# Kernel tuning notes

Hardware: AMD Instinct MI355X
Metric: run time of the kernel (lower is better)

Reference implementation:

```python
import jax, jax.numpy as jnp
import numpy as np

B, L, D, H, FF = 2, 2048, 2048, 16, 8192
DH = D // H
NEG = -1e9


def setup_inputs() -> dict:
    key = jax.random.key(0)
    ks = jax.random.split(key, 9)
    x = jax.random.normal(ks[0], (B, L, D), dtype=jnp.float32)
    # additive causal mask, broadcastable to [B, H, L, L]
    causal = jnp.triu(jnp.full((L, L), NEG, dtype=jnp.float32), k=1)
    mask = causal[None, None, :, :]
    s = 1.0 / np.sqrt(D)
    Wq = jax.random.normal(ks[1], (D, D), dtype=jnp.float32) * s
    Wk = jax.random.normal(ks[2], (D, D), dtype=jnp.float32) * s
    Wv = jax.random.normal(ks[3], (D, D), dtype=jnp.float32) * s
    Wo = jax.random.normal(ks[4], (D, D), dtype=jnp.float32) * s
    W_up = jax.random.normal(ks[5], (FF, D), dtype=jnp.float32) * s
    b_up = jnp.zeros((FF,), dtype=jnp.float32)
    W_down = jax.random.normal(ks[6], (D, FF), dtype=jnp.float32) * (1.0 / np.sqrt(FF))
    return {"x": x, "mask": mask, "Wq": Wq, "Wk": Wk, "Wv": Wv, "Wo": Wo,
            "W_up": W_up, "b_up": b_up, "W_down": W_down}


def reference(x, mask, Wq, Wk, Wv, Wo, W_up, b_up, W_down):
    b, l, d = x.shape
    # projections (torch Linear: y = x @ W.T); reshape to [B, H, L, DH]
    q = (x @ Wq.T).reshape(b, l, H, DH).transpose(0, 2, 1, 3)
    k = (x @ Wk.T).reshape(b, l, H, DH).transpose(0, 2, 1, 3)
    v = (x @ Wv.T).reshape(b, l, H, DH).transpose(0, 2, 1, 3)
    # NOTE: original module applies NO 1/sqrt(d_head) scaling
    scores = jnp.einsum('bhqd,bhkd->bhqk', q, k) + mask
    attn = jax.nn.softmax(scores, axis=-1)
    out = jnp.einsum('bhqk,bhkd->bhqd', attn, v)
    out = out.transpose(0, 2, 1, 3).reshape(b, l, d)
    x = x + out @ Wo.T
    h = jax.nn.relu(x @ W_up.T + b_up)
    return x + h @ W_down.T
```

## Files before the change

kernel.cpp:

```cpp
#include <hip/hip_runtime.h>
#include <stdint.h>

typedef _Float16 f16;
typedef __attribute__((ext_vector_type(8))) _Float16 f16x8;
typedef __attribute__((ext_vector_type(4))) _Float16 f16x4;
typedef __attribute__((ext_vector_type(4))) float f32x4;

__device__ __forceinline__ void gload16(void* lds, const void* gc) {
  void* g = const_cast<void*>(gc);
  __builtin_amdgcn_global_load_lds((__attribute__((address_space(1))) void*)g,
                                   (__attribute__((address_space(3))) void*)lds,
                                   16, 0, 0);
}

__global__ __launch_bounds__(256) void k_cast(const float* __restrict__ in,
                                              f16* __restrict__ out, int n4) {
  int stride = gridDim.x * blockDim.x;
  for (int i = blockIdx.x * blockDim.x + threadIdx.x; i < n4; i += stride) {
    float4 v = ((const float4*)in)[i];
    f16x4 o;
    o[0] = (f16)v.x; o[1] = (f16)v.y; o[2] = (f16)v.z; o[3] = (f16)v.w;
    ((f16x4*)out)[i] = o;
  }
}

__global__ __launch_bounds__(256) void k_transpose_v(const f16* __restrict__ vp,
                                                     f16* __restrict__ vt) {
  __shared__ __attribute__((aligned(16))) f16 tile[64][66];
  const int lt = blockIdx.x, dt = blockIdx.y, bh = blockIdx.z;
  const int t = threadIdx.x;
  const int r = t >> 3, c = 8 * (t & 7);
  const f16* src = vp + ((size_t)bh * 2048 + lt * 64) * 128 + dt * 64;
#pragma unroll
  for (int i = 0; i < 2; ++i) {
    union { f16x8 v; unsigned u[4]; } uu;
    uu.v = *(const f16x8*)&src[(size_t)(i * 32 + r) * 128 + c];
#pragma unroll
    for (int j = 0; j < 4; ++j)
      *(unsigned*)&tile[i * 32 + r][c + 2 * j] = uu.u[j];
  }
  __syncthreads();
  f16* dst = vt + ((size_t)bh * 128 + dt * 64) * 2048 + lt * 64;
#pragma unroll
  for (int i = 0; i < 2; ++i) {
    const int dr = i * 32 + r;
    f16x8 o;
#pragma unroll
    for (int e = 0; e < 8; ++e) o[e] = tile[c + e][dr];
    *(f16x8*)&dst[(size_t)dr * 2048 + c] = o;
  }
}

__global__ __launch_bounds__(256) void k_fuseout(const f16* __restrict__ x1b,
                                                 const float* __restrict__ p0,
                                                 const float* __restrict__ p1,
                                                 float* __restrict__ out, int n4) {
  int stride = gridDim.x * blockDim.x;
  for (int i = blockIdx.x * blockDim.x + threadIdx.x; i < n4; i += stride) {
    float4 a = ((const float4*)p0)[i];
    float4 b = ((const float4*)p1)[i];
    f16x4 xb = ((const f16x4*)x1b)[i];
    float4 o;
    o.x = (float)xb[0] + a.x + b.x;
    o.y = (float)xb[1] + a.y + b.y;
    o.z = (float)xb[2] + a.z + b.z;
    o.w = (float)xb[3] + a.w + b.w;
    ((float4*)out)[i] = o;
  }
}

template <int EPI, int SPLITOUT, int BK>
__global__ __launch_bounds__(256, 4) void gemm_nt(const f16* __restrict__ A,
                                                  const f16* __restrict__ B,
                                                  int Kit, int ld, int N,
                                                  const float* __restrict__ res,
                                                  const float* __restrict__ bias,
                                                  float* __restrict__ outf,
                                                  float* __restrict__ outf2,
                                                  f16* __restrict__ outb,
                                                  f16* __restrict__ outb_lo,
                                                  f16* __restrict__ outv) {
  constexpr int TSZ = 128 * BK;
  constexpr int CH  = 2048;
  constexpr int RPC = CH / BK;
  constexpr int NCH = 128 / RPC;
  constexpr int CW  = BK / 8;
  __shared__ __attribute__((aligned(16))) f16 As[TSZ];
  __shared__ __attribute__((aligned(16))) f16 Bs[TSZ];
  const int t = threadIdx.x;
  const int l = t & 63;
  const int w = t >> 6;
  const int wr = w >> 1, wc = w & 1;

  const int nwg = gridDim.x * gridDim.y;
  const int id = blockIdx.y * gridDim.x + blockIdx.x;
  const int sw = (id & 7) * (nwg >> 3) + (id >> 3);
  const int bn = sw % gridDim.x;
  const int bm = sw / gridDim.x;
  const int k0 = blockIdx.z * Kit;

  f32x4 acc[4][4] = {};

  const size_t aoff = (size_t)bm * 128 * ld + k0;
  const size_t boff = (size_t)bn * 128 * ld + k0;

  const int sr = t / CW;
  const int sc = 8 * (t % CW);
  const int lbase = w * 512;

  const int lr = l & 15, lq = l >> 4;
  const int nk = Kit / BK;
  for (int kt = 0; kt < nk; ++kt) {
    const size_t gbase = (size_t)kt * BK + (size_t)sr * ld + sc;
#pragma unroll
    for (int j = 0; j < NCH; ++j) {
      gload16(As + j * CH + lbase, A + aoff + (size_t)j * RPC * ld + gbase);
      gload16(Bs + j * CH + lbase, B + boff + (size_t)j * RPC * ld + gbase);
    }
    __syncthreads();
#pragma unroll
    for (int kk = 0; kk < BK / 32; ++kk) {
      f16x8 af[4], bfr[4];
#pragma unroll
      for (int m = 0; m < 4; ++m)
        af[m] = *(const f16x8*)&As[(wr * 64 + m * 16 + lr) * BK + kk * 32 + 8 * lq];
#pragma unroll
      for (int n = 0; n < 4; ++n)
        bfr[n] = *(const f16x8*)&Bs[(wc * 64 + n * 16 + lr) * BK + kk * 32 + 8 * lq];
#pragma unroll
      for (int m = 0; m < 4; ++m)
#pragma unroll
        for (int n = 0; n < 4; ++n)
          acc[m][n] = __builtin_amdgcn_mfma_f32_16x16x32_f16(af[m], bfr[n], acc[m][n], 0, 0, 0);
    }
    __syncthreads();
  }

  const size_t QKS = (size_t)8 << 20;
#pragma unroll
  for (int m = 0; m < 4; ++m) {
#pragma unroll
    for (int r = 0; r < 4; ++r) {
      const int grow = bm * 128 + wr * 64 + m * 16 + lq * 4 + r;
#pragma unroll
      for (int n = 0; n < 4; ++n) {
        const int gcol = bn * 128 + wc * 64 + n * 16 + lr;
        const float v = acc[m][n][r];
        if constexpr (EPI == 0) {
          const int which = gcol >> 11;
          const int hcol = gcol & 2047;
          const int bb = grow >> 11, ll = grow & 2047;
          const int hh = hcol >> 7, dh = hcol & 127;
          const size_t idx = ((size_t)((bb * 16 + hh) * 2048 + ll) << 7) + dh;
          const f16 hv = (f16)v;
          if (which == 2) {
            outv[idx] = hv;
          } else {
            outb[which * QKS + idx] = hv;
            if constexpr (SPLITOUT) outb_lo[which * QKS + idx] = (f16)(v - (float)hv);
          }
        } else if constexpr (EPI == 1) {
          const size_t idx = (size_t)grow * N + gcol;
          outb[idx] = (f16)(res[idx] + v);
        } else if constexpr (EPI == 2) {
          const size_t idx = (size_t)grow * N + gcol;
          outb[idx] = (f16)fmaxf(v + bias[gcol], 0.f);
        } else {
          const size_t idx = (size_t)grow * N + gcol;
          (blockIdx.z ? outf2 : outf)[idx] = v;
        }
      }
    }
  }
}

__global__ __launch_bounds__(256) void k_attn(const f16* __restrict__ q_hi,
                                              const f16* __restrict__ q_lo,
                                              const f16* __restrict__ k_hi,
                                              const f16* __restrict__ k_lo,
                                              const f16* __restrict__ vtp,
                                              f16* __restrict__ op) {
  __shared__ __attribute__((aligned(16))) f16 Ks_hi[64 * 136];
  __shared__ __attribute__((aligned(16))) f16 Ks_lo[64 * 136];
  __shared__ __attribute__((aligned(16))) f16 Vs[128 * 72];
  __shared__ __attribute__((aligned(16))) f16 Ps[4][16 * 72];
  const int t = threadIdx.x, l = t & 63, w = t >> 6;
  const int qtA = 31 - (int)blockIdx.x;
  const int qtB = (int)blockIdx.x;
  const int bh = blockIdx.y;
  const int qA0 = qtA * 64, qB0 = qtB * 64;
  const int lr = l & 15, lq = l >> 4;

  const f16* qhp = q_hi + (size_t)bh * 2048 * 128;
  const f16* qlp = q_lo + (size_t)bh * 2048 * 128;
  const f16* khp = k_hi + (size_t)bh * 2048 * 128;
  const f16* klp = k_lo + (size_t)bh * 2048 * 128;
  const f16* vhp = vtp + (size_t)bh * 128 * 2048;

  const int krow = t >> 4, kcol8 = 8 * (t & 15);
  const int vrow = t >> 3, vcol8 = 8 * (t & 7);

  f16x8 aqhA[4], aqlA[4], aqhB[4], aqlB[4];
#pragma unroll
  for (int c = 0; c < 4; ++c) {
    const size_t qiA = (size_t)(qA0 + w * 16 + lr) * 128 + c * 32 + 8 * lq;
    const size_t qiB = (size_t)(qB0 + w * 16 + lr) * 128 + c * 32 + 8 * lq;
    aqhA[c] = *(const f16x8*)&qhp[qiA];
    aqlA[c] = *(const f16x8*)&qlp[qiA];
    aqhB[c] = *(const f16x8*)&qhp[qiB];
    aqlB[c] = *(const f16x8*)&qlp[qiB];
  }

  f32x4 accA[8] = {}, accB[8] = {};
  float mrA[4], srA[4], mrB[4], srB[4];
#pragma unroll
  for (int r = 0; r < 4; ++r) {
    mrA[r] = -1e30f; srA[r] = 0.f;
    mrB[r] = -1e30f; srB[r] = 0.f;
  }

  f16x8 kregh[4], kregl[4], vreg[4];
  auto load_tile = [&](int kt) {
#pragma unroll
    for (int i = 0; i < 4; ++i) {
      const size_t ki = (size_t)(kt * 64 + i * 16 + krow) * 128 + kcol8;
      kregh[i] = *(const f16x8*)&khp[ki];
      kregl[i] = *(const f16x8*)&klp[ki];
      vreg[i] = *(const f16x8*)&vhp[(size_t)(i * 32 + vrow) * 2048 + kt * 64 + vcol8];
    }
  };
  load_tile(0);

  auto process = [&](const f16x8 (&aqh)[4], const f16x8 (&aql)[4],
                     f32x4 (&acc)[8], float (&mr)[4], float (&sr)[4],
                     int kt, int qt, int q0) {
    f32x4 s[4];
    __builtin_amdgcn_s_setprio(1);
#pragma unroll
    for (int nt = 0; nt < 4; ++nt) {
      f32x4 zh = {}, zl = {};
#pragma unroll
      for (int kc = 0; kc < 4; ++kc) {
        const int li = (nt * 16 + lr) * 136 + kc * 32 + 8 * lq;
        f16x8 bh_ = *(const f16x8*)&Ks_hi[li];
        f16x8 bl_ = *(const f16x8*)&Ks_lo[li];
        zh = __builtin_amdgcn_mfma_f32_16x16x32_f16(aqh[kc], bh_, zh, 0, 0, 0);
        zl = __builtin_amdgcn_mfma_f32_16x16x32_f16(aql[kc], bh_, zl, 0, 0, 0);
        zl = __builtin_amdgcn_mfma_f32_16x16x32_f16(aqh[kc], bl_, zl, 0, 0, 0);
      }
#pragma unroll
      for (int r = 0; r < 4; ++r) s[nt][r] = zh[r] + zl[r];
    }
    __builtin_amdgcn_s_setprio(0);
    if (kt == qt) {
#pragma unroll
      for (int nt = 0; nt < 4; ++nt)
#pragma unroll
        for (int r = 0; r < 4; ++r) {
          const int key = kt * 64 + nt * 16 + lr;
          const int qr = q0 + w * 16 + lq * 4 + r;
          if (key > qr) s[nt][r] = -1e30f;
        }
    }
    float mnew[4], scale[4], tsum[4];
#pragma unroll
    for (int r = 0; r < 4; ++r) {
      float mx = fmaxf(fmaxf(s[0][r], s[1][r]), fmaxf(s[2][r], s[3][r]));
#pragma unroll
      for (int off = 1; off < 16; off <<= 1)
        mx = fmaxf(mx, __shfl_xor(mx, off));
      mnew[r] = fmaxf(mr[r], mx);
      scale[r] = __expf(mr[r] - mnew[r]);
      mr[r] = mnew[r];
      tsum[r] = 0.f;
    }
#pragma unroll
    for (int nt = 0; nt < 4; ++nt)
#pragma unroll
      for (int r = 0; r < 4; ++r) {
        const float p = __expf(s[nt][r] - mnew[r]);
        tsum[r] += p;
        Ps[w][(lq * 4 + r) * 72 + nt * 16 + lr] = (f16)p;
      }
#pragma unroll
    for (int r = 0; r < 4; ++r) {
      float ts = tsum[r];
#pragma unroll
      for (int off = 1; off < 16; off <<= 1)
        ts += __shfl_xor(ts, off);
      sr[r] = sr[r] * scale[r] + ts;
    }
#pragma unroll
    for (int nt = 0; nt < 8; ++nt)
#pragma unroll
      for (int r = 0; r < 4; ++r)
        acc[nt][r] *= scale[r];
    __builtin_amdgcn_s_setprio(1);
#pragma unroll
    for (int kc = 0; kc < 2; ++kc) {
      f16x8 ap = *(const f16x8*)&Ps[w][lr * 72 + kc * 32 + 8 * lq];
#pragma unroll
      for (int nt = 0; nt < 8; ++nt) {
        f16x8 bv = *(const f16x8*)&Vs[(nt * 16 + lr) * 72 + kc * 32 + 8 * lq];
        acc[nt] = __builtin_amdgcn_mfma_f32_16x16x32_f16(ap, bv, acc[nt], 0, 0, 0);
      }
    }
    __builtin_amdgcn_s_setprio(0);
  };

  for (int kt = 0; kt <= qtA; ++kt) {
    __syncthreads();
#pragma unroll
    for (int i = 0; i < 4; ++i) {
      const int li = (i * 16 + krow) * 136 + kcol8;
      *(f16x8*)&Ks_hi[li] = kregh[i];
      *(f16x8*)&Ks_lo[li] = kregl[i];
      *(f16x8*)&Vs[(i * 32 + vrow) * 72 + vcol8] = vreg[i];
    }
    __syncthreads();
    if (kt < qtA) load_tile(kt + 1);
    process(aqhA, aqlA, accA, mrA, srA, kt, qtA, qA0);
    if (kt <= qtB) process(aqhB, aqlB, accB, mrB, srB, kt, qtB, qB0);
  }

  const int bb = bh >> 4, hh = bh & 15;
  auto wout = [&](f32x4 (&acc)[8], float (&sr)[4], int q0) {
#pragma unroll
    for (int r = 0; r < 4; ++r) {
      const float inv = 1.f / sr[r];
      const size_t row = (size_t)(bb * 2048 + q0 + w * 16 + lq * 4 + r);
#pragma unroll
      for (int nt = 0; nt < 8; ++nt)
        op[row * 2048 + hh * 128 + nt * 16 + lr] = (f16)(acc[nt][r] * inv);
    }
  };
  wout(accA, srA, qA0);
  wout(accB, srB, qB0);
}

extern "C" void kernel_launch(void* const* d_in, const int* in_sizes, int n_in,
                              void* d_out, int out_size, void* d_ws, size_t ws_size,
                              hipStream_t stream) {
  const float* x   = (const float*)d_in[0];
  const float* Wq  = (const float*)d_in[2];
  const float* Wk  = (const float*)d_in[3];
  const float* Wv  = (const float*)d_in[4];
  const float* Wo  = (const float*)d_in[5];
  const float* Wup = (const float*)d_in[6];
  const float* bup = (const float*)d_in[7];
  const float* Wdn = (const float*)d_in[8];
  float* out = (float*)d_out;

  const size_t M1 = 1u << 20;
  f16* W = (f16*)d_ws;
  f16* x_hi    = W + 0 * M1;
  f16* wqkv_hi = W + 8 * M1;
  f16* wo_hi   = W + 20 * M1;
  f16* wup_hi  = W + 24 * M1;
  f16* wdn_hi  = W + 40 * M1;
  f16* q_hi    = W + 56 * M1;
  f16* q_lo    = W + 72 * M1;
  f16* vp      = W + 88 * M1;
  f16* vtb     = W + 96 * M1;
  f16* x1b   = x_hi;
  float* p0  = (float*)(W + 24 * M1);
  f16* hb    = W + 56 * M1;
  float* p1  = (float*)(W + 88 * M1);
  f16* attno = vp;
  if (ws_size < (size_t)104 * M1 * sizeof(f16)) return;

  auto cg = [](size_t n4) { size_t g = (n4 + 255) / 256; return (unsigned)(g > 2048 ? 2048 : g); };
  dim3 b256(256);
  k_cast<<<cg(2 * M1), b256, 0, stream>>>(x, x_hi, (int)(2 * M1));
  k_cast<<<cg(1 * M1), b256, 0, stream>>>(Wq, wqkv_hi, (int)(1 * M1));
  k_cast<<<cg(1 * M1), b256, 0, stream>>>(Wk, wqkv_hi + 4 * M1, (int)(1 * M1));
  k_cast<<<cg(1 * M1), b256, 0, stream>>>(Wv, wqkv_hi + 8 * M1, (int)(1 * M1));
  k_cast<<<cg(1 * M1), b256, 0, stream>>>(Wo, wo_hi, (int)(1 * M1));
  k_cast<<<cg(4 * M1), b256, 0, stream>>>(Wup, wup_hi, (int)(4 * M1));
  k_cast<<<cg(4 * M1), b256, 0, stream>>>(Wdn, wdn_hi, (int)(4 * M1));

  gemm_nt<0, 1, 64><<<dim3(48, 32), b256, 0, stream>>>(
      x_hi, wqkv_hi, 2048, 2048, 6144,
      nullptr, nullptr, nullptr, nullptr, q_hi, q_lo, vp);
  k_transpose_v<<<dim3(32, 2, 32), b256, 0, stream>>>(vp, vtb);
  k_attn<<<dim3(16, 32), b256, 0, stream>>>(
      q_hi, q_lo, q_hi + 8 * M1, q_lo + 8 * M1, vtb, attno);
  gemm_nt<1, 0, 64><<<dim3(16, 32), b256, 0, stream>>>(
      attno, wo_hi, 2048, 2048, 2048,
      x, nullptr, nullptr, nullptr, x1b, nullptr, nullptr);
  gemm_nt<2, 0, 64><<<dim3(64, 32), b256, 0, stream>>>(
      x1b, wup_hi, 2048, 2048, 8192,
      nullptr, bup, nullptr, nullptr, hb, nullptr, nullptr);
  gemm_nt<3, 0, 64><<<dim3(16, 32, 2), b256, 0, stream>>>(
      hb, wdn_hi, 4096, 8192, 2048,
      nullptr, nullptr, p0, p1, nullptr, nullptr, nullptr);
  k_fuseout<<<2048, b256, 0, stream>>>(x1b, p0, p1, out, (int)(2 * M1));
}
```

Measured before the change: 840.2 us.

## Interleave dual query tiles in attention, lazy softmax rescale, batch weight casts

The attention loop now runs QK^T and PV for both query tiles (A and B) in one interleaved MFMA stream that shares each K/V LDS read, with separate P buffers per tile. This is meant to raise MFMA density and cut redundant LDS traffic. Online softmax now rescales the accumulators only when the running max grows by more than a threshold, which skips most exp and multiply work. The six weight-cast launches are merged into two multi-tensor launches to cut launch overhead. In exchange it uses more registers and LDS, and the lazy rescale lets exponentials grow up to e^8 before a rescale, which may affect f16 P precision.

```diff
diff --git a/kernel.cpp b/kernel.cpp
--- a/kernel.cpp
+++ b/kernel.cpp
@@ -15,6 +15,36 @@
 
 __global__ __launch_bounds__(256) void k_cast(const float* __restrict__ in,
                                               f16* __restrict__ out, int n4) {
+  int stride = gridDim.x * blockDim.x;
+  for (int i = blockIdx.x * blockDim.x + threadIdx.x; i < n4; i += stride) {
+    float4 v = ((const float4*)in)[i];
+    f16x4 o;
+    o[0] = (f16)v.x; o[1] = (f16)v.y; o[2] = (f16)v.z; o[3] = (f16)v.w;
+    ((f16x4*)out)[i] = o;
+  }
+}
+
+__global__ __launch_bounds__(256) void k_cast4(const float* __restrict__ s0, const float* __restrict__ s1,
+                                               const float* __restrict__ s2, const float* __restrict__ s3,
+                                               f16* __restrict__ d0, f16* __restrict__ d1,
+                                               f16* __restrict__ d2, f16* __restrict__ d3, int n4) {
+  const int which = blockIdx.y;
+  const float* in = which == 0 ? s0 : which == 1 ? s1 : which == 2 ? s2 : s3;
+  f16* out = which == 0 ? d0 : which == 1 ? d1 : which == 2 ? d2 : d3;
+  int stride = gridDim.x * blockDim.x;
+  for (int i = blockIdx.x * blockDim.x + threadIdx.x; i < n4; i += stride) {
+    float4 v = ((const float4*)in)[i];
+    f16x4 o;
+    o[0] = (f16)v.x; o[1] = (f16)v.y; o[2] = (f16)v.z; o[3] = (f16)v.w;
+    ((f16x4*)out)[i] = o;
+  }
+}
+
+__global__ __launch_bounds__(256) void k_cast2w(const float* __restrict__ s0, const float* __restrict__ s1,
+                                                f16* __restrict__ d0, f16* __restrict__ d1, int n4) {
+  const int which = blockIdx.y;
+  const float* in = which == 0 ? s0 : s1;
+  f16* out = which == 0 ? d0 : d1;
   int stride = gridDim.x * blockDim.x;
   for (int i = blockIdx.x * blockDim.x + threadIdx.x; i < n4; i += stride) {
     float4 v = ((const float4*)in)[i];
@@ -183,7 +213,8 @@
   __shared__ __attribute__((aligned(16))) f16 Ks_hi[64 * 136];
   __shared__ __attribute__((aligned(16))) f16 Ks_lo[64 * 136];
   __shared__ __attribute__((aligned(16))) f16 Vs[128 * 72];
-  __shared__ __attribute__((aligned(16))) f16 Ps[4][16 * 72];
+  __shared__ __attribute__((aligned(16))) f16 PsA[4][16 * 72];
+  __shared__ __attribute__((aligned(16))) f16 PsB[4][16 * 72];
   const int t = threadIdx.x, l = t & 63, w = t >> 6;
   const int qtA = 31 - (int)blockIdx.x;
   const int qtB = (int)blockIdx.x;
@@ -231,56 +262,43 @@
   };
   load_tile(0);
 
-  auto process = [&](const f16x8 (&aqh)[4], const f16x8 (&aql)[4],
-                     f32x4 (&acc)[8], float (&mr)[4], float (&sr)[4],
-                     int kt, int qt, int q0) {
-    f32x4 s[4];
-    __builtin_amdgcn_s_setprio(1);
-#pragma unroll
-    for (int nt = 0; nt < 4; ++nt) {
-      f32x4 zh = {}, zl = {};
-#pragma unroll
-      for (int kc = 0; kc < 4; ++kc) {
-        const int li = (nt * 16 + lr) * 136 + kc * 32 + 8 * lq;
-        f16x8 bh_ = *(const f16x8*)&Ks_hi[li];
-        f16x8 bl_ = *(const f16x8*)&Ks_lo[li];
-        zh = __builtin_amdgcn_mfma_f32_16x16x32_f16(aqh[kc], bh_, zh, 0, 0, 0);
-        zl = __builtin_amdgcn_mfma_f32_16x16x32_f16(aql[kc], bh_, zl, 0, 0, 0);
-        zl = __builtin_amdgcn_mfma_f32_16x16x32_f16(aqh[kc], bl_, zl, 0, 0, 0);
-      }
-#pragma unroll
-      for (int r = 0; r < 4; ++r) s[nt][r] = zh[r] + zl[r];
-    }
-    __builtin_amdgcn_s_setprio(0);
-    if (kt == qt) {
-#pragma unroll
-      for (int nt = 0; nt < 4; ++nt)
-#pragma unroll
-        for (int r = 0; r < 4; ++r) {
-          const int key = kt * 64 + nt * 16 + lr;
-          const int qr = q0 + w * 16 + lq * 4 + r;
-          if (key > qr) s[nt][r] = -1e30f;
-        }
-    }
-    float mnew[4], scale[4], tsum[4];
+  auto softmax = [&](f32x4 (&s)[4], f32x4 (&acc)[8], float (&mr)[4], float (&sr)[4],
+                     f16 (&Pw)[16 * 72]) {
+    float mx[4];
 #pragma unroll
     for (int r = 0; r < 4; ++r) {
-      float mx = fmaxf(fmaxf(s[0][r], s[1][r]), fmaxf(s[2][r], s[3][r]));
+      float m = fmaxf(fmaxf(s[0][r], s[1][r]), fmaxf(s[2][r], s[3][r]));
 #pragma unroll
       for (int off = 1; off < 16; off <<= 1)
-        mx = fmaxf(mx, __shfl_xor(mx, off));
-      mnew[r] = fmaxf(mr[r], mx);
-      scale[r] = __expf(mr[r] - mnew[r]);
-      mr[r] = mnew[r];
-      tsum[r] = 0.f;
-    }
+        m = fmaxf(m, __shfl_xor(m, off));
+      mx[r] = m;
+    }
+    bool grew = false;
+#pragma unroll
+    for (int r = 0; r < 4; ++r) grew = grew || (mx[r] > mr[r] + 8.f);
+    if (__any(grew)) {
+      float scale[4];
+#pragma unroll
+      for (int r = 0; r < 4; ++r) {
+        const float mnew = fmaxf(mr[r], mx[r]);
+        scale[r] = __expf(mr[r] - mnew);
+        mr[r] = mnew;
+        sr[r] *= scale[r];
+      }
+#pragma unroll
+      for (int nt = 0; nt < 8; ++nt)
+#pragma unroll
+        for (int r = 0; r < 4; ++r)
+          acc[nt][r] *= scale[r];
+    }
+    float tsum[4] = {0.f, 0.f, 0.f, 0.f};
 #pragma unroll
     for (int nt = 0; nt < 4; ++nt)
 #pragma unroll
       for (int r = 0; r < 4; ++r) {
-        const float p = __expf(s[nt][r] - mnew[r]);
+        const float p = __expf(s[nt][r] - mr[r]);
         tsum[r] += p;
-        Ps[w][(lq * 4 + r) * 72 + nt * 16 + lr] = (f16)p;
+        Pw[(lq * 4 + r) * 72 + nt * 16 + lr] = (f16)p;
       }
 #pragma unroll
     for (int r = 0; r < 4; ++r) {
@@ -288,24 +306,8 @@
 #pragma unroll
       for (int off = 1; off < 16; off <<= 1)
         ts += __shfl_xor(ts, off);
-      sr[r] = sr[r] * scale[r] + ts;
-    }
-#pragma unroll
-    for (int nt = 0; nt < 8; ++nt)
-#pragma unroll
-      for (int r = 0; r < 4; ++r)
-        acc[nt][r] *= scale[r];
-    __builtin_amdgcn_s_setprio(1);
-#pragma unroll
-    for (int kc = 0; kc < 2; ++kc) {
-      f16x8 ap = *(const f16x8*)&Ps[w][lr * 72 + kc * 32 + 8 * lq];
-#pragma unroll
-      for (int nt = 0; nt < 8; ++nt) {
-        f16x8 bv = *(const f16x8*)&Vs[(nt * 16 + lr) * 72 + kc * 32 + 8 * lq];
-        acc[nt] = __builtin_amdgcn_mfma_f32_16x16x32_f16(ap, bv, acc[nt], 0, 0, 0);
-      }
-    }
-    __builtin_amdgcn_s_setprio(0);
+      sr[r] += ts;
+    }
   };
 
   for (int kt = 0; kt <= qtA; ++kt) {
@@ -319,8 +321,67 @@
     }
     __syncthreads();
     if (kt < qtA) load_tile(kt + 1);
-    process(aqhA, aqlA, accA, mrA, srA, kt, qtA, qA0);
-    if (kt <= qtB) process(aqhB, aqlB, accB, mrB, srB, kt, qtB, qB0);
+
+    const bool doB = (kt <= qtB);
+
+    f32x4 sA[4], sB[4];
+    __builtin_amdgcn_s_setprio(1);
+#pragma unroll
+    for (int nt = 0; nt < 4; ++nt) {
+      f32x4 zhA = {}, zlA = {}, zhB = {}, zlB = {};
+#pragma unroll
+      for (int kc = 0; kc < 4; ++kc) {
+        const int li = (nt * 16 + lr) * 136 + kc * 32 + 8 * lq;
+        f16x8 bh_ = *(const f16x8*)&Ks_hi[li];
+        f16x8 bl_ = *(const f16x8*)&Ks_lo[li];
+        zhA = __builtin_amdgcn_mfma_f32_16x16x32_f16(aqhA[kc], bh_, zhA, 0, 0, 0);
+        zlA = __builtin_amdgcn_mfma_f32_16x16x32_f16(aqlA[kc], bh_, zlA, 0, 0, 0);
+        zlA = __builtin_amdgcn_mfma_f32_16x16x32_f16(aqhA[kc], bl_, zlA, 0, 0, 0);
+        if (doB) {
+          zhB = __builtin_amdgcn_mfma_f32_16x16x32_f16(aqhB[kc], bh_, zhB, 0, 0, 0);
+          zlB = __builtin_amdgcn_mfma_f32_16x16x32_f16(aqlB[kc], bh_, zlB, 0, 0, 0);
+          zlB = __builtin_amdgcn_mfma_f32_16x16x32_f16(aqhB[kc], bl_, zlB, 0, 0, 0);
+        }
+      }
+#pragma unroll
+      for (int r = 0; r < 4; ++r) {
+        sA[nt][r] = zhA[r] + zlA[r];
+        sB[nt][r] = zhB[r] + zlB[r];
+      }
+    }
+    __builtin_amdgcn_s_setprio(0);
+
+    if (kt == qtA) {
+#pragma unroll
+      for (int nt = 0; nt < 4; ++nt)
+#pragma unroll
+        for (int r = 0; r < 4; ++r)
+          if (kt * 64 + nt * 16 + lr > qA0 + w * 16 + lq * 4 + r) sA[nt][r] = -1e30f;
+    }
+    if (doB && kt == qtB) {
+#pragma unroll
+      for (int nt = 0; nt < 4; ++nt)
+#pragma unroll
+        for (int r = 0; r < 4; ++r)
+          if (kt * 64 + nt * 16 + lr > qB0 + w * 16 + lq * 4 + r) sB[nt][r] = -1e30f;
+    }
+
+    softmax(sA, accA, mrA, srA, PsA[w]);
+    if (doB) softmax(sB, accB, mrB, srB, PsB[w]);
+
+    __builtin_amdgcn_s_setprio(1);
+#pragma unroll
+    for (int kc = 0; kc < 2; ++kc) {
+      f16x8 apA = *(const f16x8*)&PsA[w][lr * 72 + kc * 32 + 8 * lq];
+      f16x8 apB = *(const f16x8*)&PsB[w][lr * 72 + kc * 32 + 8 * lq];
+#pragma unroll
+      for (int nt = 0; nt < 8; ++nt) {
+        f16x8 bv = *(const f16x8*)&Vs[(nt * 16 + lr) * 72 + kc * 32 + 8 * lq];
+        accA[nt] = __builtin_amdgcn_mfma_f32_16x16x32_f16(apA, bv, accA[nt], 0, 0, 0);
+        if (doB) accB[nt] = __builtin_amdgcn_mfma_f32_16x16x32_f16(apB, bv, accB[nt], 0, 0, 0);
+      }
+    }
+    __builtin_amdgcn_s_setprio(0);
   }
 
   const int bb = bh >> 4, hh = bh & 15;
@@ -372,12 +433,11 @@
   auto cg = [](size_t n4) { size_t g = (n4 + 255) / 256; return (unsigned)(g > 2048 ? 2048 : g); };
   dim3 b256(256);
   k_cast<<<cg(2 * M1), b256, 0, stream>>>(x, x_hi, (int)(2 * M1));
-  k_cast<<<cg(1 * M1), b256, 0, stream>>>(Wq, wqkv_hi, (int)(1 * M1));
-  k_cast<<<cg(1 * M1), b256, 0, stream>>>(Wk, wqkv_hi + 4 * M1, (int)(1 * M1));
-  k_cast<<<cg(1 * M1), b256, 0, stream>>>(Wv, wqkv_hi + 8 * M1, (int)(1 * M1));
-  k_cast<<<cg(1 * M1), b256, 0, stream>>>(Wo, wo_hi, (int)(1 * M1));
-  k_cast<<<cg(4 * M1), b256, 0, stream>>>(Wup, wup_hi, (int)(4 * M1));
-  k_cast<<<cg(4 * M1), b256, 0, stream>>>(Wdn, wdn_hi, (int)(4 * M1));
+  k_cast4<<<dim3(cg(1 * M1), 4), b256, 0, stream>>>(
+      Wq, Wk, Wv, Wo,
+      wqkv_hi, wqkv_hi + 4 * M1, wqkv_hi + 8 * M1, wo_hi, (int)(1 * M1));
+  k_cast2w<<<dim3(cg(4 * M1), 2), b256, 0, stream>>>(
+      Wup, Wdn, wup_hi, wdn_hi, (int)(4 * M1));
 
   gemm_nt<0, 1, 64><<<dim3(48, 32), b256, 0, stream>>>(
       x_hi, wqkv_hi, 2048, 2048, 6144,
```

Result: slower. 1.003 ms (+19.4%).
